# Optimization experiments

Measured on AMD Instinct MI355X. Metric: run time of the kernel, lower is better.

The kernel has to match this reference:

```python
import jax, jax.numpy as jnp
import numpy as np

N, D, H, E, K = 4096, 1024, 2048, 8, 2


def setup_inputs() -> dict:
    key = jax.random.key(0)
    ks = jax.random.split(key, 4)
    x = jax.random.normal(ks[0], (N, D), dtype=jnp.float32)
    w_gate = jax.random.normal(ks[1], (D, E), dtype=jnp.float32) * 0.02
    w1 = jax.random.normal(ks[2], (E, D, H), dtype=jnp.float32) * (1.0 / np.sqrt(D))
    b1 = jnp.zeros((E, H), dtype=jnp.float32)
    w2 = jax.random.normal(ks[3], (E, H, D), dtype=jnp.float32) * (1.0 / np.sqrt(H))
    b2 = jnp.zeros((E, D), dtype=jnp.float32)
    return {"x": x, "w_gate": w_gate, "w1": w1, "b1": b1, "w2": w2, "b2": b2}


def reference(x, w_gate, w1, b1, w2, b2):
    # --- top-k gating ---
    logits = x @ w_gate                      # [N, E]
    top_vals, top_idx = jax.lax.top_k(logits, K)   # [N, K]
    gates_k = jax.nn.softmax(top_vals, axis=-1)    # softmax over selected experts
    # scatter sparse gates into dense [N, E] combine weights (zeros off top-k)
    gates = jnp.zeros((x.shape[0], E), dtype=x.dtype)
    gates = gates.at[jnp.arange(x.shape[0])[:, None], top_idx].set(gates_k)
    # --- expert FFNs (computed densely over experts, combined sparsely) ---
    h = jax.nn.gelu(jnp.einsum('nd,edh->neh', x, w1) + b1[None])   # [N, E, H]
    y = jnp.einsum('neh,ehd->ned', h, w2) + b2[None]               # [N, E, D]
    out = jnp.einsum('ne,ned->nd', gates, y)                        # [N, D]
    return out
```

## Files before the change

### kernel.cpp

```cpp
#include <hip/hip_runtime.h>
#include <math.h>
#include <stdint.h>

#define N_TOK 4096
#define DIM   1024
#define HID   2048
#define NE    8
#define NROWS (N_TOK * 2)
#define LDST  72
#define OBST  144
#define TPT   16
#define CAP1  144
#define CAP2  72

typedef __attribute__((ext_vector_type(8))) short bf16x8;
typedef __attribute__((ext_vector_type(4))) float f32x4;

__device__ __forceinline__ unsigned short f2bf(float f) {
    union { unsigned int i; float f; } v; v.f = f;
    unsigned int u = v.i;
    return (unsigned short)((u + 0x7FFFu + ((u >> 16) & 1u)) >> 16);
}
__device__ __forceinline__ int clampi(int v, int lo, int hi) {
    return v < lo ? lo : (v > hi ? hi : v);
}
__device__ __forceinline__ void cvt8(const float* p, unsigned short* o) {
    float4 a = *(const float4*)p;
    float4 b = *(const float4*)(p + 4);
    o[0] = f2bf(a.x); o[1] = f2bf(a.y); o[2] = f2bf(a.z); o[3] = f2bf(a.w);
    o[4] = f2bf(b.x); o[5] = f2bf(b.y); o[6] = f2bf(b.z); o[7] = f2bf(b.w);
}
__device__ __forceinline__ float fast_gelu(float v) {
    float c = 0.7978845608028654f * (v + 0.044715f * v * v * v);
    float t = 1.f - 2.f / (1.f + __expf(2.f * c));
    return 0.5f * v * (1.f + t);
}
__device__ __forceinline__ void gload_lds16(const void* g, void* l) {
    __builtin_amdgcn_global_load_lds(
        (const __attribute__((address_space(1))) unsigned int*)g,
        (__attribute__((address_space(3))) unsigned int*)l,
        16, 0, 0);
}

__global__ __launch_bounds__(256) void gate_kernel(
    const float* __restrict__ x, const float* __restrict__ wg,
    unsigned short* __restrict__ top_e, float* __restrict__ top_g)
{
    int wave = threadIdx.x >> 6;
    int lane = threadIdx.x & 63;
    int n = blockIdx.x * 4 + wave;
    if (n >= N_TOK) return;
    float acc[NE];
#pragma unroll
    for (int e = 0; e < NE; e++) acc[e] = 0.f;
    const float* xrow = x + (size_t)n * DIM;
    for (int d = lane; d < DIM; d += 64) {
        float xv = xrow[d];
        float4 wa = *(const float4*)(wg + (size_t)d * NE);
        float4 wb = *(const float4*)(wg + (size_t)d * NE + 4);
        acc[0] += xv * wa.x; acc[1] += xv * wa.y;
        acc[2] += xv * wa.z; acc[3] += xv * wa.w;
        acc[4] += xv * wb.x; acc[5] += xv * wb.y;
        acc[6] += xv * wb.z; acc[7] += xv * wb.w;
    }
#pragma unroll
    for (int e = 0; e < NE; e++) {
        float v = acc[e];
#pragma unroll
        for (int off = 32; off > 0; off >>= 1) v += __shfl_xor(v, off, 64);
        acc[e] = v;
    }
    if (lane == 0) {
        int e0 = 0; float v0 = acc[0];
#pragma unroll
        for (int e = 1; e < NE; e++) if (acc[e] > v0) { v0 = acc[e]; e0 = e; }
        int e1 = (e0 == 0) ? 1 : 0; float v1 = acc[e1];
#pragma unroll
        for (int e = 0; e < NE; e++) if (e != e0 && acc[e] > v1) { v1 = acc[e]; e1 = e; }
        float s = expf(v1 - v0);
        float g0 = 1.f / (1.f + s);
        float g1 = s / (1.f + s);
        top_e[n] = (unsigned short)(e0 | (e1 << 8));
        top_g[2 * n + 0] = g0;
        top_g[2 * n + 1] = g1;
    }
}

__global__ __launch_bounds__(256) void scatter_plan_kernel(
    const unsigned short* __restrict__ top_e, const float* __restrict__ top_g,
    int* __restrict__ row_tok, float* __restrict__ row_gate,
    int* __restrict__ work1, int* __restrict__ work2)
{
    __shared__ int lpre[256][NE];
    __shared__ int etot[NE], ebase[NE];
    __shared__ int Tst[NE + 1];
    __shared__ int kept1[NE], ovb1[NE], fb1[NE + 1];
    __shared__ int kept2[NE], ovb2[NE], fb2[NE + 1];
    int t = threadIdx.x;

    unsigned long long c64 = 0ull;
    unsigned short te[TPT];
#pragma unroll
    for (int i = 0; i < TPT; i++) {
        int v = top_e[t * TPT + i];
        te[i] = (unsigned short)v;
        c64 += 1ull << ((v & 7) * 8);
        c64 += 1ull << (((v >> 8) & 7) * 8);
    }
#pragma unroll
    for (int e = 0; e < NE; e++) lpre[t][e] = (int)((c64 >> (e * 8)) & 0xFF);
    __syncthreads();

    if (t < NE) {
        int s = 0;
        for (int i = 0; i < 256; i++) { int c = lpre[i][t]; lpre[i][t] = s; s += c; }
        etot[t] = s;
    }
    __syncthreads();
    if (t == 0) {
        int b = 0, ts = 0;
#pragma unroll
        for (int e = 0; e < NE; e++) {
            ebase[e] = b; b += etot[e];
            Tst[e] = ts; ts += (etot[e] + 127) >> 7;
        }
        Tst[NE] = ts;
        int ob = 0, fs = 0;
#pragma unroll
        for (int e = 0; e < NE; e++) {
            int it = 16 * ((etot[e] + 127) >> 7);
            kept1[e] = (it < CAP1) ? it : CAP1;
            ovb1[e] = ob; ob += it - kept1[e];
            fb1[e] = fs; fs += CAP1 - kept1[e];
        }
        fb1[NE] = fs;
        ob = 0; fs = 0;
#pragma unroll
        for (int e = 0; e < NE; e++) {
            int it = 8 * ((etot[e] + 127) >> 7);
            kept2[e] = (it < CAP2) ? it : CAP2;
            ovb2[e] = ob; ob += it - kept2[e];
            fb2[e] = fs; fs += CAP2 - kept2[e];
        }
        fb2[NE] = fs;
    }
    __syncthreads();

    for (int i = t; i < NE * CAP1; i += 256) work1[i] = -1;
    for (int i = t; i < NE * CAP2; i += 256) work2[i] = -1;
    __syncthreads();

    int S = Tst[NE];
    for (int idx = t; idx < S * 16; idx += 256) {
        int s = idx >> 4, j = idx & 15;
        int e = 0;
#pragma unroll
        for (int k = 1; k < NE; k++) if (s >= Tst[k]) e = k;
        int sl = s - Tst[e];
        int gr0 = ebase[e] + sl * 128;
        int nv = etot[e] - sl * 128; if (nv > 128) nv = 128;
        int item = (gr0 << 16) | (nv << 8) | (e << 4) | j;
        int q = sl * 16 + j;
        int pos;
        if (q < kept1[e]) pos = e * CAP1 + q;
        else {
            int o = ovb1[e] + (q - kept1[e]);
            int xc = 0;
#pragma unroll
            for (int k = 1; k < NE; k++) if (o >= fb1[k]) xc = k;
            pos = xc * CAP1 + kept1[xc] + (o - fb1[xc]);
        }
        work1[clampi(pos, 0, NE * CAP1 - 1)] = item;
    }
    for (int idx = t; idx < S * 8; idx += 256) {
        int s = idx >> 3, j = idx & 7;
        int e = 0;
#pragma unroll
        for (int k = 1; k < NE; k++) if (s >= Tst[k]) e = k;
        int sl = s - Tst[e];
        int gr0 = ebase[e] + sl * 128;
        int nv = etot[e] - sl * 128; if (nv > 128) nv = 128;
        int item = (gr0 << 16) | (nv << 8) | (e << 4) | j;
        int q = sl * 8 + j;
        int pos;
        if (q < kept2[e]) pos = e * CAP2 + q;
        else {
            int o = ovb2[e] + (q - kept2[e]);
            int xc = 0;
#pragma unroll
            for (int k = 1; k < NE; k++) if (o >= fb2[k]) xc = k;
            pos = xc * CAP2 + kept2[xc] + (o - fb2[xc]);
        }
        work2[clampi(pos, 0, NE * CAP2 - 1)] = item;
    }

#pragma unroll
    for (int i = 0; i < TPT; i++) {
        int n = t * TPT + i;
        int v = te[i];
#pragma unroll
        for (int k = 0; k < 2; k++) {
            int e = (k ? (v >> 8) : v) & 7;
            int r = clampi(ebase[e] + lpre[t][e]++, 0, NROWS - 1);
            row_tok[r]  = (n << 1) | k;
            row_gate[r] = top_g[2 * n + k];
        }
    }
}

__global__ __launch_bounds__(256) void pack_x_kernel(
    const float* __restrict__ x, unsigned short* __restrict__ xb)
{
    size_t i = (size_t)(blockIdx.x * 256 + threadIdx.x) * 8;
    unsigned short o[8];
    cvt8(x + i, o);
    *(uint4*)(xb + i) = *(uint4*)o;
}

__global__ __launch_bounds__(256) void transpose_kernel(
    const float* __restrict__ in, unsigned short* __restrict__ outp, int K, int N)
{
    int e  = blockIdx.z;
    int kb = blockIdx.x;
    int nb = blockIdx.y;
    __shared__ __align__(16) unsigned short tile[64 * LDST];
    int t = threadIdx.x;

    int r = t >> 2, cq = t & 3;
    const float* sp = in + ((size_t)e * K + kb * 64 + r) * N + nb * 64 + cq * 16;
    unsigned short v[16];
    cvt8(sp, v);
    cvt8(sp + 8, v + 8);
    *(uint4*)(&tile[r * LDST + cq * 16 + 0]) = *(uint4*)(v + 0);
    *(uint4*)(&tile[r * LDST + cq * 16 + 8]) = *(uint4*)(v + 8);
    __syncthreads();

    int c = t >> 2, kq = t & 3;
    unsigned short o[16];
#pragma unroll
    for (int i = 0; i < 16; i++) o[i] = tile[(kq * 16 + i) * LDST + c];
    unsigned short* dp = outp + ((size_t)e * N + nb * 64 + c) * K + kb * 64 + kq * 16;
    *(uint4*)(dp + 0) = *(uint4*)(o + 0);
    *(uint4*)(dp + 8) = *(uint4*)(o + 8);
}

__global__ __launch_bounds__(256) void ffn1_fast5(
    const unsigned short* __restrict__ xb,
    const unsigned short* __restrict__ w1t,
    const float* __restrict__ b1,
    const int* __restrict__ work1,
    const int* __restrict__ row_tok,
    unsigned short* __restrict__ h)
{
    int lid = blockIdx.x;
    int wv = work1[(lid & 7) * CAP1 + (lid >> 3)];
    if (wv < 0) return;
    int nb     = wv & 15;
    int e      = (wv >> 4) & 7;
    int nvalid = (wv >> 8) & 0xFF;
    int gr0    = ((unsigned)wv) >> 16;

    __shared__ __align__(16) unsigned short lds[4 * 8192];
    __shared__ int ltok[128];

    int t = threadIdx.x;
    if (t < 128) {
        int rl = clampi(t, 0, nvalid - 1);
        int idx = clampi(gr0 + rl, 0, NROWS - 1);
        ltok[t] = clampi(row_tok[idx] >> 1, 0, N_TOK - 1);
    }
    __syncthreads();

    const int n0 = nb * 128;
    int w = t >> 6;
    const unsigned short* ga[4];
    const unsigned short* gb[4];
    int lofs[4];
#pragma unroll
    for (int i = 0; i < 4; i++) {
        int idx = i * 256 + t;
        int row = idx >> 3, cc = idx & 7;
        int ccs = cc ^ (row & 7);
        ga[i] = xb + (size_t)ltok[row] * DIM + ccs * 8;
        gb[i] = w1t + ((size_t)e * HID + n0 + row) * DIM + ccs * 8;
        lofs[i] = i * 2048 + w * 512;
    }

    int lane = t & 63, quad = lane >> 4, ln = lane & 15;
    int wr = w >> 1, wc = w & 1;
    int xr = ln & 7;
    f32x4 acc[4][4];
#pragma unroll
    for (int i = 0; i < 4; i++)
#pragma unroll
        for (int j = 0; j < 4; j++) acc[i][j] = (f32x4){0.f, 0.f, 0.f, 0.f};

#pragma unroll
    for (int i = 0; i < 4; i++) {
        gload_lds16(ga[i], lds + lofs[i]);
        gload_lds16(gb[i], lds + 8192 + lofs[i]);
    }
    __syncthreads();

    int cur = 0;
    for (int kt = 0; kt < DIM / 64; kt++) {
        int nxt = cur ^ 1;
        if (kt + 1 < DIM / 64) {
            int k0 = (kt + 1) * 64;
            unsigned short* dA = lds + nxt * 16384;
            unsigned short* dB = dA + 8192;
#pragma unroll
            for (int i = 0; i < 4; i++) {
                gload_lds16(ga[i] + k0, dA + lofs[i]);
                gload_lds16(gb[i] + k0, dB + lofs[i]);
            }
        }
        const unsigned short* sA = lds + cur * 16384;
        const unsigned short* sB = sA + 8192;
#pragma unroll
        for (int kk = 0; kk < 2; kk++) {
            bf16x8 af[4], bf[4];
#pragma unroll
            for (int s = 0; s < 4; s++)
                af[s] = *(const bf16x8*)(&sA[(wr * 64 + s * 16 + ln) * 64 + (((kk * 4 + quad) ^ xr) * 8)]);
#pragma unroll
            for (int s = 0; s < 4; s++)
                bf[s] = *(const bf16x8*)(&sB[(wc * 64 + s * 16 + ln) * 64 + (((kk * 4 + quad) ^ xr) * 8)]);
#pragma unroll
            for (int i = 0; i < 4; i++)
#pragma unroll
                for (int j = 0; j < 4; j++)
                    acc[i][j] = __builtin_amdgcn_mfma_f32_16x16x32_bf16(af[i], bf[j], acc[i][j], 0, 0, 0);
        }
        __syncthreads();
        cur = nxt;
    }

    unsigned short* ob = lds;
#pragma unroll
    for (int j = 0; j < 4; j++) {
        int colL = wc * 64 + j * 16 + ln;
        float bias = b1[e * HID + n0 + colL];
#pragma unroll
        for (int i = 0; i < 4; i++) {
#pragma unroll
            for (int r = 0; r < 4; r++) {
                int m = wr * 64 + i * 16 + quad * 4 + r;
                ob[m * OBST + colL] = f2bf(fast_gelu(acc[i][j][r] + bias));
            }
        }
    }
    __syncthreads();
#pragma unroll
    for (int it = 0; it < 8; it++) {
        int idx = it * 256 + t;
        int m = idx >> 4, ch = idx & 15;
        if (m < nvalid)
            *(uint4*)(h + (size_t)(gr0 + m) * HID + n0 + ch * 8) = *(const uint4*)(ob + m * OBST + ch * 8);
    }
}

__global__ __launch_bounds__(256) void ffn2_fast7(
    const unsigned short* __restrict__ h,
    const unsigned short* __restrict__ w2t,
    const float* __restrict__ b2,
    const int* __restrict__ work2,
    const int* __restrict__ row_tok,
    const float* __restrict__ row_gate,
    float* __restrict__ out,
    float* __restrict__ ybuf1)
{
    int lid = blockIdx.x;
    int wv = work2[(lid & 7) * CAP2 + (lid >> 3)];
    if (wv < 0) return;
    int nb     = wv & 15;
    int e      = (wv >> 4) & 7;
    int nvalid = (wv >> 8) & 0xFF;
    int gr0    = ((unsigned)wv) >> 16;

    __shared__ __align__(16) unsigned short lds[4 * 8192];
    __shared__ int   ltok2[128];
    __shared__ float lgate[128];

    int t = threadIdx.x;
    if (t < 128) {
        int rl = clampi(t, 0, nvalid - 1);
        int idx = clampi(gr0 + rl, 0, NROWS - 1);
        ltok2[t] = clampi(row_tok[idx], 0, 2 * N_TOK - 1);
        lgate[t] = row_gate[idx];
    }
    __syncthreads();

    const int n0 = nb * 128;
    int w = t >> 6;
    const unsigned short* ga[4];
    const unsigned short* gb[4];
    int lofs[4];
#pragma unroll
    for (int i = 0; i < 4; i++) {
        int idx = i * 256 + t;
        int row = idx >> 3, cc = idx & 7;
        int ccs = cc ^ (row & 7);
        int arow = clampi(gr0 + row, 0, NROWS - 1);
        ga[i] = h + (size_t)arow * HID + ccs * 8;
        gb[i] = w2t + ((size_t)e * DIM + n0 + row) * HID + ccs * 8;
        lofs[i] = i * 2048 + w * 512;
    }

    int lane = t & 63, quad = lane >> 4, ln = lane & 15;
    int wr = w >> 1, wc = w & 1;
    int xr = ln & 7;
    f32x4 acc[4][4];
#pragma unroll
    for (int i = 0; i < 4; i++)
#pragma unroll
        for (int j = 0; j < 4; j++) acc[i][j] = (f32x4){0.f, 0.f, 0.f, 0.f};

#pragma unroll
    for (int i = 0; i < 4; i++) {
        gload_lds16(ga[i], lds + lofs[i]);
        gload_lds16(gb[i], lds + 8192 + lofs[i]);
    }
    __syncthreads();

    int cur = 0;
    for (int kt = 0; kt < HID / 64; kt++) {
        int nxt = cur ^ 1;
        if (kt + 1 < HID / 64) {
            int k0 = (kt + 1) * 64;
            unsigned short* dA = lds + nxt * 16384;
            unsigned short* dB = dA + 8192;
#pragma unroll
            for (int i = 0; i < 4; i++) {
                gload_lds16(ga[i] + k0, dA + lofs[i]);
                gload_lds16(gb[i] + k0, dB + lofs[i]);
            }
        }
        const unsigned short* sA = lds + cur * 16384;
        const unsigned short* sB = sA + 8192;
#pragma unroll
        for (int kk = 0; kk < 2; kk++) {
            bf16x8 af[4], bf[4];
#pragma unroll
            for (int s = 0; s < 4; s++)
                af[s] = *(const bf16x8*)(&sA[(wr * 64 + s * 16 + ln) * 64 + (((kk * 4 + quad) ^ xr) * 8)]);
#pragma unroll
            for (int s = 0; s < 4; s++)
                bf[s] = *(const bf16x8*)(&sB[(wc * 64 + s * 16 + ln) * 64 + (((kk * 4 + quad) ^ xr) * 8)]);
#pragma unroll
            for (int i = 0; i < 4; i++)
#pragma unroll
                for (int j = 0; j < 4; j++)
                    acc[i][j] = __builtin_amdgcn_mfma_f32_16x16x32_bf16(af[i], bf[j], acc[i][j], 0, 0, 0);
        }
        __syncthreads();
        cur = nxt;
    }

#pragma unroll
    for (int j = 0; j < 4; j++) {
        int col = n0 + wc * 64 + j * 16 + ln;
        float bias = b2[e * DIM + col];
#pragma unroll
        for (int i = 0; i < 4; i++) {
#pragma unroll
            for (int r = 0; r < 4; r++) {
                int m = wr * 64 + i * 16 + quad * 4 + r;
                if (m < nvalid) {
                    int rt  = ltok2[m];
                    int tok = rt >> 1;
                    float vv = (acc[i][j][r] + bias) * lgate[m];
                    float* dst = (rt & 1) ? ybuf1 : out;
                    dst[(size_t)tok * DIM + col] = vv;
                }
            }
        }
    }
}

__global__ __launch_bounds__(256) void combine_kernel(
    float4* __restrict__ out4, const float4* __restrict__ y4)
{
    int i = blockIdx.x * 256 + threadIdx.x;
    float4 a = out4[i];
    float4 b = y4[i];
    out4[i] = make_float4(a.x + b.x, a.y + b.y, a.z + b.z, a.w + b.w);
}

__global__ __launch_bounds__(256) void zero_out_kernel(float* __restrict__ out) {
    int i = blockIdx.x * 256 + threadIdx.x;
    out[i] = 0.f;
}

extern "C" void kernel_launch(void* const* d_in, const int* in_sizes, int n_in,
                              void* d_out, int out_size, void* d_ws, size_t ws_size,
                              hipStream_t stream) {
    const float* x  = (const float*)d_in[0];
    const float* wg = (const float*)d_in[1];
    const float* w1 = (const float*)d_in[2];
    const float* b1 = (const float*)d_in[3];
    const float* w2 = (const float*)d_in[4];
    const float* b2 = (const float*)d_in[5];
    float* out = (float*)d_out;

    char* ws = (char*)d_ws;
    unsigned short* top_e    = (unsigned short*)(ws + 256);
    float*          top_g    = (float*)(ws + 8448);
    int*            row_tok  = (int*)(ws + 41216);
    float*          row_gate = (float*)(ws + 73984);
    int*            work1    = (int*)(ws + 106752);
    int*            work2    = (int*)(ws + 111360);

    const size_t WT_OFF    = (size_t)1 << 17;
    const size_t HBUF_OFF  = WT_OFF + (size_t)NE * DIM * HID * 2;
    const size_t YBUF_OFF  = HBUF_OFF + (size_t)NROWS * HID * 2;
    const size_t NEEDED    = YBUF_OFF + (size_t)N_TOK * DIM * 4;

    if (ws_size < NEEDED) {
        zero_out_kernel<<<dim3(N_TOK * DIM / 256), dim3(256), 0, stream>>>(out);
        return;
    }

    unsigned short* wt    = (unsigned short*)(ws + WT_OFF);
    unsigned short* hbuf  = (unsigned short*)(ws + HBUF_OFF);
    float*          ybuf1 = (float*)(ws + YBUF_OFF);
    unsigned short* xb    = (unsigned short*)(ws + YBUF_OFF);

    gate_kernel<<<dim3(N_TOK / 4), dim3(256), 0, stream>>>(x, wg, top_e, top_g);
    scatter_plan_kernel<<<dim3(1), dim3(256), 0, stream>>>(top_e, top_g, row_tok, row_gate, work1, work2);
    pack_x_kernel<<<dim3(N_TOK * DIM / (256 * 8)), dim3(256), 0, stream>>>(x, xb);
    transpose_kernel<<<dim3(DIM / 64, HID / 64, NE), dim3(256), 0, stream>>>(w1, wt, DIM, HID);
    ffn1_fast5<<<dim3(NE * CAP1), dim3(256), 0, stream>>>(xb, wt, b1, work1, row_tok, hbuf);
    transpose_kernel<<<dim3(HID / 64, DIM / 64, NE), dim3(256), 0, stream>>>(w2, wt, HID, DIM);
    ffn2_fast7<<<dim3(NE * CAP2), dim3(256), 0, stream>>>(hbuf, wt, b2, work2, row_tok, row_gate, out, ybuf1);
    combine_kernel<<<dim3(N_TOK * DIM / 1024), dim3(256), 0, stream>>>((float4*)out, (const float4*)ybuf1);
}
```

Baseline: 369.4 us.

## Drop LDS double buffering in expert GEMMs to raise occupancy

Both expert FFN GEMM kernels go from a two-stage double-buffered LDS pipeline to a single buffer: load a K tile, sync, compute, sync. This halves per-block shared memory from 64KB to 32KB so more blocks fit on each CU. The epilogue staging stride shrinks from 144 to 128 so the output tile still fits in the smaller buffer. The cost is that prefetch no longer overlaps compute inside a block, so latency hiding depends on other resident blocks, and the unpadded epilogue stride may add LDS bank conflicts.

Result: no change. 374.7 us (+1.4%).

```diff
diff --git a/kernel.cpp b/kernel.cpp
--- a/kernel.cpp
+++ b/kernel.cpp
@@ -8,7 +8,7 @@
 #define NE    8
 #define NROWS (N_TOK * 2)
 #define LDST  72
-#define OBST  144
+#define OBST  128
 #define TPT   16
 #define CAP1  144
 #define CAP2  72
@@ -244,7 +244,7 @@
     *(uint4*)(dp + 8) = *(uint4*)(o + 8);
 }
 
-__global__ __launch_bounds__(256) void ffn1_fast5(
+__global__ __launch_bounds__(256) void ffn1_fast6(
     const unsigned short* __restrict__ xb,
     const unsigned short* __restrict__ w1t,
     const float* __restrict__ b1,
@@ -260,7 +260,7 @@
     int nvalid = (wv >> 8) & 0xFF;
     int gr0    = ((unsigned)wv) >> 16;
 
-    __shared__ __align__(16) unsigned short lds[4 * 8192];
+    __shared__ __align__(16) unsigned short lds[2 * 8192];
     __shared__ int ltok[128];
 
     int t = threadIdx.x;
@@ -295,37 +295,23 @@
 #pragma unroll
         for (int j = 0; j < 4; j++) acc[i][j] = (f32x4){0.f, 0.f, 0.f, 0.f};
 
-#pragma unroll
-    for (int i = 0; i < 4; i++) {
-        gload_lds16(ga[i], lds + lofs[i]);
-        gload_lds16(gb[i], lds + 8192 + lofs[i]);
-    }
-    __syncthreads();
-
-    int cur = 0;
     for (int kt = 0; kt < DIM / 64; kt++) {
-        int nxt = cur ^ 1;
-        if (kt + 1 < DIM / 64) {
-            int k0 = (kt + 1) * 64;
-            unsigned short* dA = lds + nxt * 16384;
-            unsigned short* dB = dA + 8192;
-#pragma unroll
-            for (int i = 0; i < 4; i++) {
-                gload_lds16(ga[i] + k0, dA + lofs[i]);
-                gload_lds16(gb[i] + k0, dB + lofs[i]);
-            }
-        }
-        const unsigned short* sA = lds + cur * 16384;
-        const unsigned short* sB = sA + 8192;
+        int k0 = kt * 64;
+#pragma unroll
+        for (int i = 0; i < 4; i++) {
+            gload_lds16(ga[i] + k0, lds + lofs[i]);
+            gload_lds16(gb[i] + k0, lds + 8192 + lofs[i]);
+        }
+        __syncthreads();
 #pragma unroll
         for (int kk = 0; kk < 2; kk++) {
             bf16x8 af[4], bf[4];
 #pragma unroll
             for (int s = 0; s < 4; s++)
-                af[s] = *(const bf16x8*)(&sA[(wr * 64 + s * 16 + ln) * 64 + (((kk * 4 + quad) ^ xr) * 8)]);
+                af[s] = *(const bf16x8*)(&lds[(wr * 64 + s * 16 + ln) * 64 + (((kk * 4 + quad) ^ xr) * 8)]);
 #pragma unroll
             for (int s = 0; s < 4; s++)
-                bf[s] = *(const bf16x8*)(&sB[(wc * 64 + s * 16 + ln) * 64 + (((kk * 4 + quad) ^ xr) * 8)]);
+                bf[s] = *(const bf16x8*)(&lds[8192 + (wc * 64 + s * 16 + ln) * 64 + (((kk * 4 + quad) ^ xr) * 8)]);
 #pragma unroll
             for (int i = 0; i < 4; i++)
 #pragma unroll
@@ -333,7 +319,6 @@
                     acc[i][j] = __builtin_amdgcn_mfma_f32_16x16x32_bf16(af[i], bf[j], acc[i][j], 0, 0, 0);
         }
         __syncthreads();
-        cur = nxt;
     }
 
     unsigned short* ob = lds;
@@ -360,7 +345,7 @@
     }
 }
 
-__global__ __launch_bounds__(256) void ffn2_fast7(
+__global__ __launch_bounds__(256) void ffn2_fast8(
     const unsigned short* __restrict__ h,
     const unsigned short* __restrict__ w2t,
     const float* __restrict__ b2,
@@ -378,7 +363,7 @@
     int nvalid = (wv >> 8) & 0xFF;
     int gr0    = ((unsigned)wv) >> 16;
 
-    __shared__ __align__(16) unsigned short lds[4 * 8192];
+    __shared__ __align__(16) unsigned short lds[2 * 8192];
     __shared__ int   ltok2[128];
     __shared__ float lgate[128];
 
@@ -416,37 +401,23 @@
 #pragma unroll
         for (int j = 0; j < 4; j++) acc[i][j] = (f32x4){0.f, 0.f, 0.f, 0.f};
 
-#pragma unroll
-    for (int i = 0; i < 4; i++) {
-        gload_lds16(ga[i], lds + lofs[i]);
-        gload_lds16(gb[i], lds + 8192 + lofs[i]);
-    }
-    __syncthreads();
-
-    int cur = 0;
     for (int kt = 0; kt < HID / 64; kt++) {
-        int nxt = cur ^ 1;
-        if (kt + 1 < HID / 64) {
-            int k0 = (kt + 1) * 64;
-            unsigned short* dA = lds + nxt * 16384;
-            unsigned short* dB = dA + 8192;
-#pragma unroll
-            for (int i = 0; i < 4; i++) {
-                gload_lds16(ga[i] + k0, dA + lofs[i]);
-                gload_lds16(gb[i] + k0, dB + lofs[i]);
-            }
-        }
-        const unsigned short* sA = lds + cur * 16384;
-        const unsigned short* sB = sA + 8192;
+        int k0 = kt * 64;
+#pragma unroll
+        for (int i = 0; i < 4; i++) {
+            gload_lds16(ga[i] + k0, lds + lofs[i]);
+            gload_lds16(gb[i] + k0, lds + 8192 + lofs[i]);
+        }
+        __syncthreads();
 #pragma unroll
         for (int kk = 0; kk < 2; kk++) {
             bf16x8 af[4], bf[4];
 #pragma unroll
             for (int s = 0; s < 4; s++)
-                af[s] = *(const bf16x8*)(&sA[(wr * 64 + s * 16 + ln) * 64 + (((kk * 4 + quad) ^ xr) * 8)]);
+                af[s] = *(const bf16x8*)(&lds[(wr * 64 + s * 16 + ln) * 64 + (((kk * 4 + quad) ^ xr) * 8)]);
 #pragma unroll
             for (int s = 0; s < 4; s++)
-                bf[s] = *(const bf16x8*)(&sB[(wc * 64 + s * 16 + ln) * 64 + (((kk * 4 + quad) ^ xr) * 8)]);
+                bf[s] = *(const bf16x8*)(&lds[8192 + (wc * 64 + s * 16 + ln) * 64 + (((kk * 4 + quad) ^ xr) * 8)]);
 #pragma unroll
             for (int i = 0; i < 4; i++)
 #pragma unroll
@@ -454,7 +425,6 @@
                     acc[i][j] = __builtin_amdgcn_mfma_f32_16x16x32_bf16(af[i], bf[j], acc[i][j], 0, 0, 0);
         }
         __syncthreads();
-        cur = nxt;
     }
 
 #pragma unroll
@@ -530,8 +500,8 @@
     scatter_plan_kernel<<<dim3(1), dim3(256), 0, stream>>>(top_e, top_g, row_tok, row_gate, work1, work2);
     pack_x_kernel<<<dim3(N_TOK * DIM / (256 * 8)), dim3(256), 0, stream>>>(x, xb);
     transpose_kernel<<<dim3(DIM / 64, HID / 64, NE), dim3(256), 0, stream>>>(w1, wt, DIM, HID);
-    ffn1_fast5<<<dim3(NE * CAP1), dim3(256), 0, stream>>>(xb, wt, b1, work1, row_tok, hbuf);
+    ffn1_fast6<<<dim3(NE * CAP1), dim3(256), 0, stream>>>(xb, wt, b1, work1, row_tok, hbuf);
     transpose_kernel<<<dim3(HID / 64, DIM / 64, NE), dim3(256), 0, stream>>>(w2, wt, HID, DIM);
-    ffn2_fast7<<<dim3(NE * CAP2), dim3(256), 0, stream>>>(hbuf, wt, b2, work2, row_tok, row_gate, out, ybuf1);
+    ffn2_fast8<<<dim3(NE * CAP2), dim3(256), 0, stream>>>(hbuf, wt, b2, work2, row_tok, row_gate, out, ybuf1);
     combine_kernel<<<dim3(N_TOK * DIM / 1024), dim3(256), 0, stream>>>((float4*)out, (const float4*)ybuf1);
 }
```
